# Kernel optimization log

Hardware: AMD Instinct MI355X
Metric: run time of the kernel (lower is better)

The kernel has to match this reference:

```python
import jax, jax.numpy as jnp
import numpy as np

N = 64      # num_agents
Z = 512     # z_dim
D = 512     # d_model


def setup_inputs() -> dict:
    key = jax.random.key(0)
    k0, k1, k2, k3, k4 = jax.random.split(key, 5)
    z = jax.random.normal(k0, (N, Z), dtype=jnp.float32)
    # per-agent unshared projections (bias=False), kaiming-uniform-ish scale
    s = 1.0 / np.sqrt(Z).astype(np.float32)
    Wq = jax.random.normal(k1, (N, D, Z), dtype=jnp.float32) * s
    Wk = jax.random.normal(k2, (N, D, Z), dtype=jnp.float32) * s
    Wv = jax.random.normal(k3, (N, D, Z), dtype=jnp.float32) * s
    Wi = jax.random.normal(k4, (Z, D), dtype=jnp.float32) * (1.0 / np.sqrt(D).astype(np.float32))
    bi = jnp.zeros((Z,), dtype=jnp.float32)
    return {"z": z, "Wq": Wq, "Wk": Wk, "Wv": Wv, "Wi": Wi, "bi": bi}


def reference(z, Wq, Wk, Wv, Wi, bi):
    n, d = z.shape[0], Wq.shape[1]
    scale = jnp.sqrt(jnp.asarray(d, z.dtype))
    # batched per-agent GEMV: Q[n] = Wq[n] @ z[n]
    Q = jnp.einsum('ndz,nz->nd', Wq, z)
    K = jnp.einsum('ndz,nz->nd', Wk, z)
    V = jnp.einsum('ndz,nz->nd', Wv, z)
    # S[i, j] = <K_i, Q_j> / sqrt(d); complete graph minus self-edges
    S = (K @ Q.T) / scale
    S = jnp.where(jnp.eye(n, dtype=bool), -jnp.inf, S)
    alpha = jax.nn.softmax(S, axis=0)            # softmax over senders i for each receiver j
    messages = jnp.einsum('ij,id->jd', alpha, V)  # (N, D)
    # infer aux loss: each sender i is inferred identically by all N-1 receivers,
    # so the mean over N*(N-1) pairs equals the mean over i of per-agent MSE.
    hat = V @ Wi.T + bi                           # (N, Z)
    per_agent_mse = jnp.mean((hat - z) ** 2, axis=1)
    total_infer_loss = jnp.mean(per_agent_mse)
    return messages, total_infer_loss
```

## Files before the change

### kernel.cpp

```cpp
#include <hip/hip_runtime.h>
#include <math.h>

#define NAG 64
#define ZD  512
#define DM  512

__device__ __forceinline__ float dot8(float4 wa, float4 wb, float4 za, float4 zb)
{
    return wa.x*za.x + wa.y*za.y + wa.z*za.z + wa.w*za.w
         + wb.x*zb.x + wb.y*zb.y + wb.z*zb.z + wb.w*zb.w;
}

#define LDG4(dst, ptr) dst = *reinterpret_cast<const float4*>(ptr)

__global__ __launch_bounds__(256, 3) void qkv_gemv_kernel(
    const float* __restrict__ z,
    const float* __restrict__ Wq,
    const float* __restrict__ Wk,
    const float* __restrict__ Wv,
    float* __restrict__ Q, float* __restrict__ K, float* __restrict__ V)
{
    const int wave = threadIdx.x >> 6;
    const int lane = threadIdx.x & 63;
    const int gw   = blockIdx.x * 4 + wave;
    const int rb   = gw * 32;
    const int m    = rb >> 15;
    const int n    = (rb >> 9) & 63;
    const int d0   = rb & 511;

    const float* __restrict__ Wm = ((m == 0) ? Wq : (m == 1) ? Wk : Wv)
                                   + ((size_t)(n * DM + d0)) * ZD;
    float* __restrict__ O        = ((m == 0) ? Q : (m == 1) ? K : V)
                                   + n * DM + d0;
    const float* __restrict__ zn = z + n * ZD;

    const int lo = lane * 4;
    const int hi = 256 + lane * 4;

    const float4 za = *reinterpret_cast<const float4*>(zn + lo);
    const float4 zb = *reinterpret_cast<const float4*>(zn + hi);

    float4 c0, c1, c2, c3, c4, c5, c6, c7;
    {
        const float* b = Wm;
        LDG4(c0, b + lo);            LDG4(c1, b + hi);
        LDG4(c2, b + ZD + lo);       LDG4(c3, b + ZD + hi);
        LDG4(c4, b + 2 * ZD + lo);   LDG4(c5, b + 2 * ZD + hi);
        LDG4(c6, b + 3 * ZD + lo);   LDG4(c7, b + 3 * ZD + hi);
    }

#pragma unroll
    for (int g = 0; g < 8; ++g) {
        float4 n0, n1, n2, n3, n4, n5, n6, n7;
        if (g < 7) {
            const float* b = Wm + (size_t)(g + 1) * 4 * ZD;
            LDG4(n0, b + lo);            LDG4(n1, b + hi);
            LDG4(n2, b + ZD + lo);       LDG4(n3, b + ZD + hi);
            LDG4(n4, b + 2 * ZD + lo);   LDG4(n5, b + 2 * ZD + hi);
            LDG4(n6, b + 3 * ZD + lo);   LDG4(n7, b + 3 * ZD + hi);
        }
        __builtin_amdgcn_sched_barrier(0);

        float a0 = dot8(c0, c1, za, zb);
        float a1 = dot8(c2, c3, za, zb);
        float a2 = dot8(c4, c5, za, zb);
        float a3 = dot8(c6, c7, za, zb);
#pragma unroll
        for (int off = 32; off > 0; off >>= 1) {
            a0 += __shfl_down(a0, off);
            a1 += __shfl_down(a1, off);
            a2 += __shfl_down(a2, off);
            a3 += __shfl_down(a3, off);
        }
        if (lane == 0)
            *reinterpret_cast<float4*>(O + g * 4) = make_float4(a0, a1, a2, a3);

        if (g < 7) {
            c0 = n0; c1 = n1; c2 = n2; c3 = n3;
            c4 = n4; c5 = n5; c6 = n6; c7 = n7;
        }
    }
}

__global__ __launch_bounds__(256) void attn_infer_kernel(
    const float* __restrict__ Q, const float* __restrict__ K,
    const float* __restrict__ V, const float* __restrict__ Wi,
    const float* __restrict__ bi, const float* __restrict__ z,
    float* __restrict__ out, float* __restrict__ zp_partial)
{
    __shared__ __align__(16) float sbuf[DM];
    __shared__ float Sc[NAG];
    __shared__ float Al[NAG];
    const int t = threadIdx.x;

    if (blockIdx.x < NAG) {
        const int j = blockIdx.x;
        sbuf[t]       = Q[j * DM + t];
        sbuf[t + 256] = Q[j * DM + t + 256];
        __syncthreads();

        const int i = t >> 2;
        const int c = t & 3;
        const float* Krow = K + i * DM + c * 128;
        const float* Qsub = sbuf + c * 128;
        float p = 0.f;
#pragma unroll
        for (int k = 0; k < 32; ++k) {
            float4 kv = *reinterpret_cast<const float4*>(Krow + k * 4);
            float4 qv = *reinterpret_cast<const float4*>(Qsub + k * 4);
            p += kv.x*qv.x + kv.y*qv.y + kv.z*qv.z + kv.w*qv.w;
        }
        p += __shfl_xor(p, 1);
        p += __shfl_xor(p, 2);
        if (c == 0)
            Sc[i] = (i == j) ? -INFINITY : p * 0.044194173824159216f;
        __syncthreads();

        if (t < 64) {
            float s = Sc[t];
            float mx = s;
#pragma unroll
            for (int off = 32; off > 0; off >>= 1) mx = fmaxf(mx, __shfl_xor(mx, off));
            float e = expf(s - mx);
            float sum = e;
#pragma unroll
            for (int off = 32; off > 0; off >>= 1) sum += __shfl_xor(sum, off);
            Al[t] = e / sum;
        }
        __syncthreads();

#pragma unroll
        for (int dd = 0; dd < 2; ++dd) {
            const int d = t + dd * 256;
            float acc = 0.f;
            for (int i2 = 0; i2 < NAG; ++i2) acc += Al[i2] * V[i2 * DM + d];
            out[j * DM + d] = acc;
        }
    } else {
        const int zp = blockIdx.x - NAG;
        const float* wr = Wi + (size_t)zp * DM;
        sbuf[t]       = wr[t];
        sbuf[t + 256] = wr[t + 256];
        __syncthreads();

        const int i = t >> 2;
        const int c = t & 3;
        const float* Vrow = V + i * DM + c * 128;
        const float* Wsub = sbuf + c * 128;
        float p = 0.f;
#pragma unroll
        for (int k = 0; k < 32; ++k) {
            float4 vv = *reinterpret_cast<const float4*>(Vrow + k * 4);
            float4 wv = *reinterpret_cast<const float4*>(Wsub + k * 4);
            p += vv.x*wv.x + vv.y*wv.y + vv.z*wv.z + vv.w*wv.w;
        }
        p += __shfl_xor(p, 1);
        p += __shfl_xor(p, 2);

        float e2 = 0.f;
        if (c == 0) {
            float e = p + bi[zp] - z[i * ZD + zp];
            e2 = e * e;
        }
#pragma unroll
        for (int off = 32; off > 0; off >>= 1) e2 += __shfl_down(e2, off);

        const int wv2 = t >> 6;
        const int ln  = t & 63;
        if (ln == 0) Sc[wv2] = e2;
        __syncthreads();
        if (t == 0) zp_partial[zp] = Sc[0] + Sc[1] + Sc[2] + Sc[3];
    }
}

__global__ __launch_bounds__(64) void loss_reduce_kernel(
    const float* __restrict__ zp_partial, float* __restrict__ out)
{
    float v = 0.f;
#pragma unroll
    for (int k = 0; k < 8; ++k) v += zp_partial[threadIdx.x + k * 64];
#pragma unroll
    for (int off = 32; off > 0; off >>= 1) v += __shfl_down(v, off);
    if (threadIdx.x == 0) out[NAG * DM] = v * (1.0f / (NAG * ZD));
}

extern "C" void kernel_launch(void* const* d_in, const int* in_sizes, int n_in,
                              void* d_out, int out_size, void* d_ws, size_t ws_size,
                              hipStream_t stream) {
    const float* z  = (const float*)d_in[0];
    const float* Wq = (const float*)d_in[1];
    const float* Wk = (const float*)d_in[2];
    const float* Wv = (const float*)d_in[3];
    const float* Wi = (const float*)d_in[4];
    const float* bi = (const float*)d_in[5];
    float* out = (float*)d_out;

    float* Q = (float*)d_ws;
    float* K = Q + NAG * DM;
    float* V = K + NAG * DM;
    float* partial = V + NAG * DM;

    hipLaunchKernelGGL(qkv_gemv_kernel, dim3(768), dim3(256), 0, stream,
                       z, Wq, Wk, Wv, Q, K, V);
    hipLaunchKernelGGL(attn_infer_kernel, dim3(NAG + ZD), dim3(256), 0, stream,
                       Q, K, V, Wi, bi, z, out, partial);
    hipLaunchKernelGGL(loss_reduce_kernel, dim3(1), dim3(64), 0, stream,
                       partial, out);
}
```

Before: 56.50 us.

## Double-buffer QKV GEMV weight loads with inline asm and explicit vmcnt waits

Rewrites the QKV GEMV inner loop to use inline-asm global_load_dwordx4 with immediate offsets and two register buffers (A/B), so two groups of 4 rows are in flight while the previous group is computed. Explicit s_waitcnt vmcnt(8) waits replace compiler-managed waits, keeping more memory requests outstanding in this bandwidth-bound kernel. It raises register pressure and relies on hand-written waitcnt correctness; the COMPUTE macro also writes a float4 store that the compiler may not count against vmcnt ordering.

```diff
diff --git a/kernel.cpp b/kernel.cpp
--- a/kernel.cpp
+++ b/kernel.cpp
@@ -5,13 +5,47 @@
 #define ZD  512
 #define DM  512
 
-__device__ __forceinline__ float dot8(float4 wa, float4 wb, float4 za, float4 zb)
-{
-    return wa.x*za.x + wa.y*za.y + wa.z*za.z + wa.w*za.w
-         + wb.x*zb.x + wb.y*zb.y + wb.z*zb.z + wb.w*zb.w;
-}
-
-#define LDG4(dst, ptr) dst = *reinterpret_cast<const float4*>(ptr)
+typedef float f32x4 __attribute__((ext_vector_type(4)));
+
+#define GLD(d, b, OFF) \
+    asm volatile("global_load_dwordx4 %0, %1, off offset:" OFF \
+                 : "=v"(d) : "v"(b))
+
+#define VWAIT(N) do { \
+    asm volatile("s_waitcnt vmcnt(" #N ")" ::: "memory"); \
+    __builtin_amdgcn_sched_barrier(0); \
+} while (0)
+
+#define ISSUE(P, base) do { \
+    const float* _bA = (base); \
+    const float* _bC = _bA + 2 * ZD; \
+    GLD(P##0, _bA, "0");    GLD(P##1, _bA, "1024"); \
+    GLD(P##2, _bA, "2048"); GLD(P##3, _bA, "3072"); \
+    GLD(P##4, _bC, "0");    GLD(P##5, _bC, "1024"); \
+    GLD(P##6, _bC, "2048"); GLD(P##7, _bC, "3072"); \
+} while (0)
+
+__device__ __forceinline__ float dot8v(f32x4 wa, f32x4 wb, f32x4 za, f32x4 zb)
+{
+    return wa[0]*za[0] + wa[1]*za[1] + wa[2]*za[2] + wa[3]*za[3]
+         + wb[0]*zb[0] + wb[1]*zb[1] + wb[2]*zb[2] + wb[3]*zb[3];
+}
+
+#define COMPUTE(P, g) do { \
+    float a0 = dot8v(P##0, P##1, zA, zB); \
+    float a1 = dot8v(P##2, P##3, zA, zB); \
+    float a2 = dot8v(P##4, P##5, zA, zB); \
+    float a3 = dot8v(P##6, P##7, zA, zB); \
+    _Pragma("unroll") \
+    for (int off = 32; off > 0; off >>= 1) { \
+        a0 += __shfl_down(a0, off); \
+        a1 += __shfl_down(a1, off); \
+        a2 += __shfl_down(a2, off); \
+        a3 += __shfl_down(a3, off); \
+    } \
+    if (lane == 0) \
+        *reinterpret_cast<float4*>(O + (g) * 4) = make_float4(a0, a1, a2, a3); \
+} while (0)
 
 __global__ __launch_bounds__(256, 3) void qkv_gemv_kernel(
     const float* __restrict__ z,
@@ -34,52 +68,26 @@
                                    + n * DM + d0;
     const float* __restrict__ zn = z + n * ZD;
 
-    const int lo = lane * 4;
-    const int hi = 256 + lane * 4;
-
-    const float4 za = *reinterpret_cast<const float4*>(zn + lo);
-    const float4 zb = *reinterpret_cast<const float4*>(zn + hi);
-
-    float4 c0, c1, c2, c3, c4, c5, c6, c7;
-    {
-        const float* b = Wm;
-        LDG4(c0, b + lo);            LDG4(c1, b + hi);
-        LDG4(c2, b + ZD + lo);       LDG4(c3, b + ZD + hi);
-        LDG4(c4, b + 2 * ZD + lo);   LDG4(c5, b + 2 * ZD + hi);
-        LDG4(c6, b + 3 * ZD + lo);   LDG4(c7, b + 3 * ZD + hi);
-    }
-
-#pragma unroll
-    for (int g = 0; g < 8; ++g) {
-        float4 n0, n1, n2, n3, n4, n5, n6, n7;
-        if (g < 7) {
-            const float* b = Wm + (size_t)(g + 1) * 4 * ZD;
-            LDG4(n0, b + lo);            LDG4(n1, b + hi);
-            LDG4(n2, b + ZD + lo);       LDG4(n3, b + ZD + hi);
-            LDG4(n4, b + 2 * ZD + lo);   LDG4(n5, b + 2 * ZD + hi);
-            LDG4(n6, b + 3 * ZD + lo);   LDG4(n7, b + 3 * ZD + hi);
-        }
-        __builtin_amdgcn_sched_barrier(0);
-
-        float a0 = dot8(c0, c1, za, zb);
-        float a1 = dot8(c2, c3, za, zb);
-        float a2 = dot8(c4, c5, za, zb);
-        float a3 = dot8(c6, c7, za, zb);
-#pragma unroll
-        for (int off = 32; off > 0; off >>= 1) {
-            a0 += __shfl_down(a0, off);
-            a1 += __shfl_down(a1, off);
-            a2 += __shfl_down(a2, off);
-            a3 += __shfl_down(a3, off);
-        }
-        if (lane == 0)
-            *reinterpret_cast<float4*>(O + g * 4) = make_float4(a0, a1, a2, a3);
-
-        if (g < 7) {
-            c0 = n0; c1 = n1; c2 = n2; c3 = n3;
-            c4 = n4; c5 = n5; c6 = n6; c7 = n7;
-        }
-    }
+    const float* lp = Wm + lane * 4;
+    const float* zp = zn + lane * 4;
+
+    f32x4 zA, zB;
+    f32x4 A0, A1, A2, A3, A4, A5, A6, A7;
+    f32x4 B0, B1, B2, B3, B4, B5, B6, B7;
+
+    GLD(zA, zp, "0");
+    GLD(zB, zp, "1024");
+    ISSUE(A, lp);
+    ISSUE(B, lp + 4 * ZD);
+
+    VWAIT(8);  COMPUTE(A, 0);  ISSUE(A, lp +  8 * ZD);
+    VWAIT(8);  COMPUTE(B, 1);  ISSUE(B, lp + 12 * ZD);
+    VWAIT(8);  COMPUTE(A, 2);  ISSUE(A, lp + 16 * ZD);
+    VWAIT(8);  COMPUTE(B, 3);  ISSUE(B, lp + 20 * ZD);
+    VWAIT(8);  COMPUTE(A, 4);  ISSUE(A, lp + 24 * ZD);
+    VWAIT(8);  COMPUTE(B, 5);  ISSUE(B, lp + 28 * ZD);
+    VWAIT(8);  COMPUTE(A, 6);
+    VWAIT(0);  COMPUTE(B, 7);
 }
 
 __global__ __launch_bounds__(256) void attn_infer_kernel(
```

After: 53.70 us. 1.05x faster.
